# Kernel tuning notes

Measured on AMD Instinct MI355X. Metric: run time of the kernel, lower is better.

Reference implementation:

```python
import jax, jax.numpy as jnp
import numpy as np

N_NODES = 50000
N_EDGES = 200000


def _glorot(key, shape):
    fan_in, fan_out = shape[0], shape[1]
    lim = np.sqrt(6.0 / (fan_in + fan_out))
    return jax.random.uniform(key, shape, jnp.float32, -lim, lim)


def setup_inputs() -> dict:
    key = jax.random.key(0)
    ks = jax.random.split(key, 20)
    x = jax.random.normal(ks[0], (N_NODES, 2), jnp.float32)
    edge_index = jax.random.randint(ks[1], (2, N_EDGES), 0, N_NODES, jnp.int64)
    edge_attr = jax.random.uniform(ks[2], (N_EDGES, 2), jnp.float32)
    # conv1: NNConv(2 -> 32), edge nn: Linear(2,16) -> ReLU -> Linear(16, 2*32)
    nn1_w1 = _glorot(ks[3], (2, 16)); nn1_b1 = jnp.zeros((16,), jnp.float32)
    nn1_w2 = _glorot(ks[4], (16, 64)); nn1_b2 = jnp.zeros((64,), jnp.float32)
    root1 = _glorot(ks[5], (2, 32)); bias1 = jnp.zeros((32,), jnp.float32)
    # conv2: NNConv(32 -> 32), edge nn: Linear(2,16) -> ReLU -> Linear(16, 1024)
    nn2_w1 = _glorot(ks[6], (2, 16)); nn2_b1 = jnp.zeros((16,), jnp.float32)
    nn2_w2 = _glorot(ks[7], (16, 1024)); nn2_b2 = jnp.zeros((1024,), jnp.float32)
    root2 = _glorot(ks[8], (32, 32)); bias2 = jnp.zeros((32,), jnp.float32)
    # fc2: Linear(32 -> 1)  (fc1 is unused in the original forward)
    fc2_w = _glorot(ks[9], (32, 1)); fc2_b = jnp.zeros((1,), jnp.float32)
    return dict(x=x, edge_index=edge_index, edge_attr=edge_attr,
                nn1_w1=nn1_w1, nn1_b1=nn1_b1, nn1_w2=nn1_w2, nn1_b2=nn1_b2,
                root1=root1, bias1=bias1,
                nn2_w1=nn2_w1, nn2_b1=nn2_b1, nn2_w2=nn2_w2, nn2_b2=nn2_b2,
                root2=root2, bias2=bias2, fc2_w=fc2_w, fc2_b=fc2_b)


def _nnconv(x, src, dst, edge_attr, w1, b1, w2, b2, root, bias, in_ch, out_ch):
    # per-edge weight matrices from edge MLP: [E, in_ch*out_ch]
    h = jax.nn.relu(edge_attr @ w1 + b1) @ w2 + b2
    W = h.reshape(-1, in_ch, out_ch)               # [E, in, out]
    msg = jnp.einsum('ei,eio->eo', x[src], W)      # gather + per-edge matvec
    agg = jax.ops.segment_sum(msg, dst, num_segments=x.shape[0])  # scatter-add
    return agg + x @ root + bias                   # add aggr + root transform


def reference(x, edge_index, edge_attr,
              nn1_w1, nn1_b1, nn1_w2, nn1_b2, root1, bias1,
              nn2_w1, nn2_b1, nn2_w2, nn2_b2, root2, bias2,
              fc2_w, fc2_b):
    src, dst = edge_index[0], edge_index[1]
    h = jax.nn.relu(_nnconv(x, src, dst, edge_attr,
                            nn1_w1, nn1_b1, nn1_w2, nn1_b2, root1, bias1, 2, 32))
    h = jax.nn.relu(_nnconv(h, src, dst, edge_attr,
                            nn2_w1, nn2_b1, nn2_w2, nn2_b2, root2, bias2, 32, 32))
    return h @ fc2_w + fc2_b  # [N, 1]
```

## Files before the change

kernel.cpp:

```cpp
#include <hip/hip_runtime.h>
#include <hip/hip_bf16.h>


typedef __attribute__((ext_vector_type(8))) short short8;
typedef __attribute__((ext_vector_type(4))) float f32x4;

union frag_u { short8 s; unsigned u[4]; };

__device__ inline unsigned cvt_pk2(float lo, float hi) {
    union { __hip_bfloat162 h; unsigned u; } c;
    c.h = __float22bfloat162_rn(make_float2(lo, hi));
    return c.u;
}

__global__ __launch_bounds__(256, 4) void edge2_mfma(
    const float* __restrict__ h1,
    const int*   __restrict__ ei,
    const float* __restrict__ ea,
    const float* __restrict__ w1,
    const float* __restrict__ b1,
    const float* __restrict__ w2,
    const float* __restrict__ b2,
    float* __restrict__ agg,
    int E)
{
    const int tid  = threadIdx.x;
    const int lane = tid & 63;
    const int wv   = tid >> 6;
    const int nh   = wv & 1;
    const int gsel = wv >> 1;
    const int r16  = lane & 15;
    const int g    = lane >> 4;
    const int oo   = nh * 16 + r16;
    const int g8   = g * 8;

    short8 bfrag[17];
#pragma unroll
    for (int t = 0; t < 16; ++t) {
        frag_u f;
#pragma unroll
        for (int wd = 0; wd < 4; ++wd) {
            int i0 = g8 + 2 * wd;
            f.u[wd] = cvt_pk2(w2[t * 1024 + i0 * 32 + oo],
                              w2[t * 1024 + (i0 + 1) * 32 + oo]);
        }
        bfrag[t] = f.s;
    }
    {
        frag_u f;
#pragma unroll
        for (int wd = 0; wd < 4; ++wd) {
            int i0 = g8 + 2 * wd;
            f.u[wd] = cvt_pk2(b2[i0 * 32 + oo], b2[(i0 + 1) * 32 + oo]);
        }
        bfrag[16] = f.s;
    }

    float w1r0[16], w1r1[16], b1r[16];
#pragma unroll
    for (int k = 0; k < 16; ++k) {
        w1r0[k] = w1[k]; w1r1[k] = w1[16 + k]; b1r[k] = b1[k];
    }

    const int pairs = (E + 31) >> 5;
    for (int p = blockIdx.x; p < pairs; p += gridDim.x) {
        const int base = p * 32 + gsel * 16;
        const int edge = base + r16;
        const bool ev = edge < E;
        const int ec = ev ? edge : 0;

        int    src = ei[ec];
        float2 eav = *(const float2*)(ea + 2 * (size_t)ec);
        float4 hA  = *(const float4*)(h1 + (size_t)src * 32 + g8);
        float4 hB  = *(const float4*)(h1 + (size_t)src * 32 + g8 + 4);
        if (!ev) { hA = make_float4(0.f,0.f,0.f,0.f); hB = make_float4(0.f,0.f,0.f,0.f); }

        float he[16];
#pragma unroll
        for (int k = 0; k < 16; ++k) {
            float v = fmaf(eav.x, w1r0[k], fmaf(eav.y, w1r1[k], b1r[k]));
            he[k] = v > 0.f ? v : 0.f;
        }

        f32x4 acc = {0.f, 0.f, 0.f, 0.f};
#pragma unroll
        for (int t = 0; t < 16; ++t) {
            frag_u a;
            a.u[0] = cvt_pk2(he[t] * hA.x, he[t] * hA.y);
            a.u[1] = cvt_pk2(he[t] * hA.z, he[t] * hA.w);
            a.u[2] = cvt_pk2(he[t] * hB.x, he[t] * hB.y);
            a.u[3] = cvt_pk2(he[t] * hB.z, he[t] * hB.w);
            acc = __builtin_amdgcn_mfma_f32_16x16x32_bf16(a.s, bfrag[t], acc, 0, 0, 0);
        }
        {
            frag_u a;
            a.u[0] = cvt_pk2(hA.x, hA.y);
            a.u[1] = cvt_pk2(hA.z, hA.w);
            a.u[2] = cvt_pk2(hB.x, hB.y);
            a.u[3] = cvt_pk2(hB.z, hB.w);
            acc = __builtin_amdgcn_mfma_f32_16x16x32_bf16(a.s, bfrag[16], acc, 0, 0, 0);
        }

        float* ap = agg + oo;
        if (base + g * 4 + 3 < E) {
            int4 d4 = *(const int4*)(ei + (size_t)E + base + g * 4);
            atomicAdd(ap + (size_t)d4.x * 32, acc[0]);
            atomicAdd(ap + (size_t)d4.y * 32, acc[1]);
            atomicAdd(ap + (size_t)d4.z * 32, acc[2]);
            atomicAdd(ap + (size_t)d4.w * 32, acc[3]);
        } else {
#pragma unroll
            for (int j = 0; j < 4; ++j) {
                int eg = base + g * 4 + j;
                if (eg < E) atomicAdd(ap + (size_t)ei[E + eg] * 32, acc[j]);
            }
        }
    }
}

__global__ __launch_bounds__(256, 4) void edge1_mfma(
    const float* __restrict__ x,
    const int*   __restrict__ ei,
    const float* __restrict__ ea,
    const float* __restrict__ w1,
    const float* __restrict__ b1,
    const float* __restrict__ w2,
    const float* __restrict__ b2,
    float* __restrict__ agg,
    int E)
{
    const int tid  = threadIdx.x;
    const int lane = tid & 63;
    const int wv   = tid >> 6;
    const int nh   = wv & 1;
    const int gsel = wv >> 1;
    const int r16  = lane & 15;
    const int g    = lane >> 4;
    const int oo   = nh * 16 + r16;
    const int g8   = g * 8;

    short8 bf0, bf1;
    {
        frag_u f;
#pragma unroll
        for (int wd = 0; wd < 4; ++wd) {
            int kk0 = g8 + 2 * wd, kk1 = kk0 + 1;
            f.u[wd] = cvt_pk2(w2[(kk0 >> 1) * 64 + (kk0 & 1) * 32 + oo],
                              w2[(kk1 >> 1) * 64 + (kk1 & 1) * 32 + oo]);
        }
        bf0 = f.s;
        f.u[0] = (g == 0) ? cvt_pk2(b2[oo], b2[32 + oo]) : 0u;
        f.u[1] = 0u; f.u[2] = 0u; f.u[3] = 0u;
        bf1 = f.s;
    }

    const float4 w1a = *(const float4*)(w1 + g * 4);
    const float4 w1b = *(const float4*)(w1 + 16 + g * 4);
    const float4 b1v = *(const float4*)(b1 + g * 4);

    const int pairs = (E + 31) >> 5;
    for (int p = blockIdx.x; p < pairs; p += gridDim.x) {
        const int base = p * 32 + gsel * 16;
        const int edge = base + r16;
        const bool ev = edge < E;
        const int ec = ev ? edge : 0;

        int    src = ei[ec];
        float2 eav = *(const float2*)(ea + 2 * (size_t)ec);
        float2 xv  = *(const float2*)(x + 2 * (size_t)src);
        if (!ev) xv = make_float2(0.f, 0.f);

        float he0 = fmaf(eav.x, w1a.x, fmaf(eav.y, w1b.x, b1v.x)); he0 = he0 > 0.f ? he0 : 0.f;
        float he1 = fmaf(eav.x, w1a.y, fmaf(eav.y, w1b.y, b1v.y)); he1 = he1 > 0.f ? he1 : 0.f;
        float he2 = fmaf(eav.x, w1a.z, fmaf(eav.y, w1b.z, b1v.z)); he2 = he2 > 0.f ? he2 : 0.f;
        float he3 = fmaf(eav.x, w1a.w, fmaf(eav.y, w1b.w, b1v.w)); he3 = he3 > 0.f ? he3 : 0.f;

        frag_u a;
        a.u[0] = cvt_pk2(he0 * xv.x, he0 * xv.y);
        a.u[1] = cvt_pk2(he1 * xv.x, he1 * xv.y);
        a.u[2] = cvt_pk2(he2 * xv.x, he2 * xv.y);
        a.u[3] = cvt_pk2(he3 * xv.x, he3 * xv.y);
        f32x4 acc = {0.f, 0.f, 0.f, 0.f};
        acc = __builtin_amdgcn_mfma_f32_16x16x32_bf16(a.s, bf0, acc, 0, 0, 0);

        a.u[0] = (g == 0) ? cvt_pk2(xv.x, xv.y) : 0u;
        a.u[1] = 0u; a.u[2] = 0u; a.u[3] = 0u;
        acc = __builtin_amdgcn_mfma_f32_16x16x32_bf16(a.s, bf1, acc, 0, 0, 0);

        float* ap = agg + oo;
        if (base + g * 4 + 3 < E) {
            int4 d4 = *(const int4*)(ei + (size_t)E + base + g * 4);
            atomicAdd(ap + (size_t)d4.x * 32, acc[0]);
            atomicAdd(ap + (size_t)d4.y * 32, acc[1]);
            atomicAdd(ap + (size_t)d4.z * 32, acc[2]);
            atomicAdd(ap + (size_t)d4.w * 32, acc[3]);
        } else {
#pragma unroll
            for (int j = 0; j < 4; ++j) {
                int eg = base + g * 4 + j;
                if (eg < E) atomicAdd(ap + (size_t)ei[E + eg] * 32, acc[j]);
            }
        }
    }
}

__global__ __launch_bounds__(256) void node1_kernel(
    const float* __restrict__ x, const float* __restrict__ agg,
    const float* __restrict__ root, const float* __restrict__ bias,
    float* __restrict__ h1, int N)
{
    int gid = blockIdx.x * blockDim.x + threadIdx.x;
    int n = gid >> 5, o = gid & 31;
    if (n >= N) return;
    float v = agg[(size_t)n * 32 + o]
            + x[2 * n] * root[o] + x[2 * n + 1] * root[32 + o] + bias[o];
    h1[(size_t)n * 32 + o] = v > 0.f ? v : 0.f;
}

__global__ __launch_bounds__(256) void node2_kernel(
    const float* __restrict__ h1, const float* __restrict__ agg,
    const float* __restrict__ root2, const float* __restrict__ bias2,
    const float* __restrict__ fc2w, const float* __restrict__ fc2b,
    float* __restrict__ out, int N)
{
    __shared__ float s_r[1024];
    for (int t = threadIdx.x; t < 1024; t += blockDim.x) s_r[t] = root2[t];
    __syncthreads();

    int gid = blockIdx.x * blockDim.x + threadIdx.x;
    int n = gid >> 5, o = gid & 31;
    if (n >= N) return;

    float mine = h1[(size_t)n * 32 + o];
    float v = agg[(size_t)n * 32 + o] + bias2[o];
#pragma unroll
    for (int i = 0; i < 32; ++i) {
        float hi = __shfl(mine, i, 32);
        v = fmaf(hi, s_r[i * 32 + o], v);
    }
    v = v > 0.f ? v : 0.f;
    v *= fc2w[o];
#pragma unroll
    for (int off = 16; off; off >>= 1) v += __shfl_xor(v, off, 32);
    if (o == 0) out[n] = v + fc2b[0];
}

extern "C" void kernel_launch(void* const* d_in, const int* in_sizes, int n_in,
                              void* d_out, int out_size, void* d_ws, size_t ws_size,
                              hipStream_t stream) {
    const float* x      = (const float*)d_in[0];
    const int*   ei     = (const int*)  d_in[1];
    const float* ea     = (const float*)d_in[2];
    const float* nn1_w1 = (const float*)d_in[3];
    const float* nn1_b1 = (const float*)d_in[4];
    const float* nn1_w2 = (const float*)d_in[5];
    const float* nn1_b2 = (const float*)d_in[6];
    const float* root1  = (const float*)d_in[7];
    const float* bias1  = (const float*)d_in[8];
    const float* nn2_w1 = (const float*)d_in[9];
    const float* nn2_b1 = (const float*)d_in[10];
    const float* nn2_w2 = (const float*)d_in[11];
    const float* nn2_b2 = (const float*)d_in[12];
    const float* root2  = (const float*)d_in[13];
    const float* bias2  = (const float*)d_in[14];
    const float* fc2w   = (const float*)d_in[15];
    const float* fc2b   = (const float*)d_in[16];

    const int N = in_sizes[0] / 2;
    const int E = in_sizes[2] / 2;

    float* agg1 = (float*)d_ws;
    float* agg2 = agg1 + (size_t)N * 32;
    float* h1   = agg2 + (size_t)N * 32;

    hipMemsetAsync(d_ws, 0, (size_t)N * 64 * sizeof(float), stream);

    edge1_mfma<<<1024, 256, 0, stream>>>(
        x, ei, ea, nn1_w1, nn1_b1, nn1_w2, nn1_b2, agg1, E);

    node1_kernel<<<(N * 32 + 255) / 256, 256, 0, stream>>>(
        x, agg1, root1, bias1, h1, N);

    edge2_mfma<<<1024, 256, 0, stream>>>(
        h1, ei, ea, nn2_w1, nn2_b1, nn2_w2, nn2_b2, agg2, E);

    node2_kernel<<<(N * 32 + 255) / 256, 256, 0, stream>>>(
        h1, agg2, root2, bias2, fc2w, fc2b, (float*)d_out, N);
}
```

Measured before the change: 169.9 us.

## Fuse node1 into edge2 and node2, prefetch next edge indices

Removes the node1 kernel and the h1 buffer. Layer-1 root transform, bias and ReLU are now recomputed per edge from agg1 and x inside edge2, and per node inside node2. edge2 also software-prefetches the next iteration's src index, edge attributes and destination indices. Launch bounds drop to 3 blocks/SM and the grid to 768 blocks. This saves one launch and the h1 write/read pass, at the cost of redundant per-edge layer-1 arithmetic, an extra x gather per edge, more register pressure and lower occupancy.

Result: no change. 168.5 us (-0.8%).

```diff
diff --git a/kernel.cpp b/kernel.cpp
--- a/kernel.cpp
+++ b/kernel.cpp
@@ -12,11 +12,15 @@
     c.h = __float22bfloat162_rn(make_float2(lo, hi));
     return c.u;
 }
-
-__global__ __launch_bounds__(256, 4) void edge2_mfma(
-    const float* __restrict__ h1,
+__device__ inline float relu(float v) { return v > 0.f ? v : 0.f; }
+
+__global__ __launch_bounds__(256, 3) void edge2_fused(
+    const float* __restrict__ x,
+    const float* __restrict__ agg1,
     const int*   __restrict__ ei,
     const float* __restrict__ ea,
+    const float* __restrict__ root1,
+    const float* __restrict__ bias1,
     const float* __restrict__ w1,
     const float* __restrict__ b1,
     const float* __restrict__ w2,
@@ -56,6 +60,13 @@
         bfrag[16] = f.s;
     }
 
+    const float4 r0a = *(const float4*)(root1 + g8);
+    const float4 r0b = *(const float4*)(root1 + g8 + 4);
+    const float4 r1a = *(const float4*)(root1 + 32 + g8);
+    const float4 r1b = *(const float4*)(root1 + 32 + g8 + 4);
+    const float4 b1a = *(const float4*)(bias1 + g8);
+    const float4 b1b = *(const float4*)(bias1 + g8 + 4);
+
     float w1r0[16], w1r1[16], b1r[16];
 #pragma unroll
     for (int k = 0; k < 16; ++k) {
@@ -63,24 +74,49 @@
     }
 
     const int pairs = (E + 31) >> 5;
-    for (int p = blockIdx.x; p < pairs; p += gridDim.x) {
-        const int base = p * 32 + gsel * 16;
-        const int edge = base + r16;
-        const bool ev = edge < E;
-        const int ec = ev ? edge : 0;
-
-        int    src = ei[ec];
-        float2 eav = *(const float2*)(ea + 2 * (size_t)ec);
-        float4 hA  = *(const float4*)(h1 + (size_t)src * 32 + g8);
-        float4 hB  = *(const float4*)(h1 + (size_t)src * 32 + g8 + 4);
+    int p = blockIdx.x;
+    if (p >= pairs) return;
+
+    int base_c = p * 32 + gsel * 16;
+    int ec     = min(base_c + r16, E - 1);
+    int    src_c = ei[ec];
+    float2 ea_c  = *(const float2*)(ea + 2 * (size_t)ec);
+    int4   d4_c  = *(const int4*)(ei + (size_t)E + min(base_c + g * 4, E - 4));
+
+    for (; p < pairs; p += gridDim.x) {
+        const int base = base_c;
+        const bool ev  = (base + r16) < E;
+
+        float2 xv = *(const float2*)(x + 2 * (size_t)src_c);
+        float4 aA = *(const float4*)(agg1 + (size_t)src_c * 32 + g8);
+        float4 aB = *(const float4*)(agg1 + (size_t)src_c * 32 + g8 + 4);
+        float2 eav = ea_c;
+        int4   d4  = d4_c;
+
+        int pn = p + gridDim.x;
+        if (pn < pairs) {
+            base_c = pn * 32 + gsel * 16;
+            int ecn = min(base_c + r16, E - 1);
+            src_c = ei[ecn];
+            ea_c  = *(const float2*)(ea + 2 * (size_t)ecn);
+            d4_c  = *(const int4*)(ei + (size_t)E + min(base_c + g * 4, E - 4));
+        }
+
+        float4 hA, hB;
+        hA.x = relu(aA.x + xv.x * r0a.x + xv.y * r1a.x + b1a.x);
+        hA.y = relu(aA.y + xv.x * r0a.y + xv.y * r1a.y + b1a.y);
+        hA.z = relu(aA.z + xv.x * r0a.z + xv.y * r1a.z + b1a.z);
+        hA.w = relu(aA.w + xv.x * r0a.w + xv.y * r1a.w + b1a.w);
+        hB.x = relu(aB.x + xv.x * r0b.x + xv.y * r1b.x + b1b.x);
+        hB.y = relu(aB.y + xv.x * r0b.y + xv.y * r1b.y + b1b.y);
+        hB.z = relu(aB.z + xv.x * r0b.z + xv.y * r1b.z + b1b.z);
+        hB.w = relu(aB.w + xv.x * r0b.w + xv.y * r1b.w + b1b.w);
         if (!ev) { hA = make_float4(0.f,0.f,0.f,0.f); hB = make_float4(0.f,0.f,0.f,0.f); }
 
         float he[16];
 #pragma unroll
-        for (int k = 0; k < 16; ++k) {
-            float v = fmaf(eav.x, w1r0[k], fmaf(eav.y, w1r1[k], b1r[k]));
-            he[k] = v > 0.f ? v : 0.f;
-        }
+        for (int k = 0; k < 16; ++k)
+            he[k] = relu(fmaf(eav.x, w1r0[k], fmaf(eav.y, w1r1[k], b1r[k])));
 
         f32x4 acc = {0.f, 0.f, 0.f, 0.f};
 #pragma unroll
@@ -103,7 +139,6 @@
 
         float* ap = agg + oo;
         if (base + g * 4 + 3 < E) {
-            int4 d4 = *(const int4*)(ei + (size_t)E + base + g * 4);
             atomicAdd(ap + (size_t)d4.x * 32, acc[0]);
             atomicAdd(ap + (size_t)d4.y * 32, acc[1]);
             atomicAdd(ap + (size_t)d4.z * 32, acc[2]);
@@ -170,10 +205,10 @@
         float2 xv  = *(const float2*)(x + 2 * (size_t)src);
         if (!ev) xv = make_float2(0.f, 0.f);
 
-        float he0 = fmaf(eav.x, w1a.x, fmaf(eav.y, w1b.x, b1v.x)); he0 = he0 > 0.f ? he0 : 0.f;
-        float he1 = fmaf(eav.x, w1a.y, fmaf(eav.y, w1b.y, b1v.y)); he1 = he1 > 0.f ? he1 : 0.f;
-        float he2 = fmaf(eav.x, w1a.z, fmaf(eav.y, w1b.z, b1v.z)); he2 = he2 > 0.f ? he2 : 0.f;
-        float he3 = fmaf(eav.x, w1a.w, fmaf(eav.y, w1b.w, b1v.w)); he3 = he3 > 0.f ? he3 : 0.f;
+        float he0 = relu(fmaf(eav.x, w1a.x, fmaf(eav.y, w1b.x, b1v.x)));
+        float he1 = relu(fmaf(eav.x, w1a.y, fmaf(eav.y, w1b.y, b1v.y)));
+        float he2 = relu(fmaf(eav.x, w1a.z, fmaf(eav.y, w1b.z, b1v.z)));
+        float he3 = relu(fmaf(eav.x, w1a.w, fmaf(eav.y, w1b.w, b1v.w)));
 
         frag_u a;
         a.u[0] = cvt_pk2(he0 * xv.x, he0 * xv.y);
@@ -204,24 +239,18 @@
     }
 }
 
-__global__ __launch_bounds__(256) void node1_kernel(
-    const float* __restrict__ x, const float* __restrict__ agg,
-    const float* __restrict__ root, const float* __restrict__ bias,
-    float* __restrict__ h1, int N)
-{
-    int gid = blockIdx.x * blockDim.x + threadIdx.x;
-    int n = gid >> 5, o = gid & 31;
-    if (n >= N) return;
-    float v = agg[(size_t)n * 32 + o]
-            + x[2 * n] * root[o] + x[2 * n + 1] * root[32 + o] + bias[o];
-    h1[(size_t)n * 32 + o] = v > 0.f ? v : 0.f;
-}
-
-__global__ __launch_bounds__(256) void node2_kernel(
-    const float* __restrict__ h1, const float* __restrict__ agg,
-    const float* __restrict__ root2, const float* __restrict__ bias2,
-    const float* __restrict__ fc2w, const float* __restrict__ fc2b,
-    float* __restrict__ out, int N)
+__global__ __launch_bounds__(256) void node2_fused(
+    const float* __restrict__ x,
+    const float* __restrict__ agg1,
+    const float* __restrict__ agg2,
+    const float* __restrict__ root1,
+    const float* __restrict__ bias1,
+    const float* __restrict__ root2,
+    const float* __restrict__ bias2,
+    const float* __restrict__ fc2w,
+    const float* __restrict__ fc2b,
+    float* __restrict__ out,
+    int N)
 {
     __shared__ float s_r[1024];
     for (int t = threadIdx.x; t < 1024; t += blockDim.x) s_r[t] = root2[t];
@@ -231,14 +260,17 @@
     int n = gid >> 5, o = gid & 31;
     if (n >= N) return;
 
-    float mine = h1[(size_t)n * 32 + o];
-    float v = agg[(size_t)n * 32 + o] + bias2[o];
+    float2 xv = *(const float2*)(x + 2 * (size_t)n);
+    float h1o = relu(agg1[(size_t)n * 32 + o]
+                   + xv.x * root1[o] + xv.y * root1[32 + o] + bias1[o]);
+
+    float v = agg2[(size_t)n * 32 + o] + bias2[o];
 #pragma unroll
     for (int i = 0; i < 32; ++i) {
-        float hi = __shfl(mine, i, 32);
+        float hi = __shfl(h1o, i, 32);
         v = fmaf(hi, s_r[i * 32 + o], v);
     }
-    v = v > 0.f ? v : 0.f;
+    v = relu(v);
     v *= fc2w[o];
 #pragma unroll
     for (int off = 16; off; off >>= 1) v += __shfl_xor(v, off, 32);
@@ -271,19 +303,17 @@
 
     float* agg1 = (float*)d_ws;
     float* agg2 = agg1 + (size_t)N * 32;
-    float* h1   = agg2 + (size_t)N * 32;
 
     hipMemsetAsync(d_ws, 0, (size_t)N * 64 * sizeof(float), stream);
 
     edge1_mfma<<<1024, 256, 0, stream>>>(
         x, ei, ea, nn1_w1, nn1_b1, nn1_w2, nn1_b2, agg1, E);
 
-    node1_kernel<<<(N * 32 + 255) / 256, 256, 0, stream>>>(
-        x, agg1, root1, bias1, h1, N);
-
-    edge2_mfma<<<1024, 256, 0, stream>>>(
-        h1, ei, ea, nn2_w1, nn2_b1, nn2_w2, nn2_b2, agg2, E);
-
-    node2_kernel<<<(N * 32 + 255) / 256, 256, 0, stream>>>(
-        h1, agg2, root2, bias2, fc2w, fc2b, (float*)d_out, N);
-}
+    edge2_fused<<<768, 256, 0, stream>>>(
+        x, agg1, ei, ea, root1, bias1,
+        nn2_w1, nn2_b1, nn2_w2, nn2_b2, agg2, E);
+
+    node2_fused<<<(N * 32 + 255) / 256, 256, 0, stream>>>(
+        x, agg1, agg2, root1, bias1, root2, bias2, fc2w, fc2b,
+        (float*)d_out, N);
+}
```
